# Optimization experiments

Hardware: AMD Instinct MI355X
Metric: run time of the kernel (lower is better)

## Reference

```python
import jax, jax.numpy as jnp
import numpy as np

B, S, H = 1, 2048, 2048
HD, NQ, NKV = 128, 16, 4
FFH = 8192
EPS = 1e-5
ROPE_BASE = 10000.0
SOFTMAX_CAP = 50.0
CLIP_L, CLIP_R = 0.0, 1.0


def setup_inputs() -> dict:
    key = jax.random.key(0)
    ks = jax.random.split(key, 10)
    std = 0.02
    return {
        "x": jax.random.normal(ks[0], (B, S, H), dtype=jnp.float32),
        "attn_norm_w": jax.random.uniform(ks[1], (H,), minval=-1.0, maxval=1.0, dtype=jnp.float32),
        "mlp_norm_w": jax.random.uniform(ks[2], (H,), minval=-1.0, maxval=1.0, dtype=jnp.float32),
        "wq": jax.random.normal(ks[3], (H, NQ * HD), dtype=jnp.float32) * std,
        "wk": jax.random.normal(ks[4], (H, NKV * HD), dtype=jnp.float32) * std,
        "wv": jax.random.normal(ks[5], (H, NKV * HD), dtype=jnp.float32) * std,
        "wo": jax.random.normal(ks[6], (NQ * HD, H), dtype=jnp.float32) * std,
        "w_gate": jax.random.normal(ks[7], (H, FFH), dtype=jnp.float32) * std,
        "w_up": jax.random.normal(ks[8], (H, FFH), dtype=jnp.float32) * std,
        "w_down": jax.random.normal(ks[9], (FFH, H), dtype=jnp.float32) * std,
    }


def _rms_norm(x, w):
    # GroupRMSNorm with group_size=None -> whole hidden dim
    var = jnp.mean(jnp.square(x), axis=-1, keepdims=True)
    return x * jax.lax.rsqrt(var + EPS) * w


def _rope_cos_sin(seq_len, dim):
    inv_freq = 1.0 / (ROPE_BASE ** (jnp.arange(0, dim, 2, dtype=jnp.float32) / dim))
    t = jnp.arange(seq_len, dtype=jnp.float32)
    freqs = jnp.outer(t, inv_freq)                      # [S, dim/2]
    emb = jnp.concatenate([freqs, freqs], axis=-1)      # [S, dim]
    return jnp.cos(emb), jnp.sin(emb)


def _apply_rope(x, cos, sin):
    # x: [B, S, h, d]; rotate-half (LLaMA-style)
    d = x.shape[-1]
    x1, x2 = x[..., : d // 2], x[..., d // 2 :]
    rot = jnp.concatenate([-x2, x1], axis=-1)
    return x * cos[None, :, None, :] + rot * sin[None, :, None, :]


def _qk_norm(x):
    # per-head RMS norm over head_dim (qk_norm_group_size == head_dim), unit weight
    var = jnp.mean(jnp.square(x), axis=-1, keepdims=True)
    return x * jax.lax.rsqrt(var + EPS)


def reference(x, attn_norm_w, mlp_norm_w, wq, wk, wv, wo, w_gate, w_up, w_down):
    # ---- attention sub-layer ----
    h = _rms_norm(x, attn_norm_w)                                     # [B,S,H]
    q = (h @ wq).reshape(B, S, NQ, HD)
    k = (h @ wk).reshape(B, S, NKV, HD)
    v = (h @ wv).reshape(B, S, NKV, HD)

    cos, sin = _rope_cos_sin(S, HD)
    q = _apply_rope(q, cos, sin)
    k = _apply_rope(k, cos, sin)

    q = _qk_norm(q)
    k = _qk_norm(k)

    # GQA: expand kv heads to match q heads
    rep = NQ // NKV
    k = jnp.repeat(k, rep, axis=2)                                    # [B,S,NQ,HD]
    v = jnp.repeat(v, rep, axis=2)

    scale = 1.0 / jnp.sqrt(jnp.float32(HD))
    scores = jnp.einsum("bshd,bthd->bhst", q, k) * scale              # [B,NQ,S,S]
    # softmax cap: cap * tanh(s / cap)
    scores = SOFTMAX_CAP * jnp.tanh(scores / SOFTMAX_CAP)
    causal = jnp.tril(jnp.ones((S, S), dtype=bool))
    scores = jnp.where(causal[None, None], scores, -jnp.inf)
    p = jax.nn.softmax(scores, axis=-1)
    # clip range (l, r): clamp(p * (r - l) + l, 0, 1)
    p = jnp.clip(p * (CLIP_R - CLIP_L) + CLIP_L, 0.0, 1.0)
    o = jnp.einsum("bhst,bthd->bshd", p, v).reshape(B, S, NQ * HD)
    x = x + o @ wo

    # ---- MLP sub-layer (gated SiLU) ----
    h2 = _rms_norm(x, mlp_norm_w)
    mlp_out = (jax.nn.silu(h2 @ w_gate) * (h2 @ w_up)) @ w_down
    return x + mlp_out
```

## Files before the change

kernel.cpp:

```cpp
#include <hip/hip_runtime.h>

typedef __bf16 bf16;
typedef __bf16 bf16x4 __attribute__((ext_vector_type(4)));
typedef __bf16 bf16x8 __attribute__((ext_vector_type(8)));
typedef float f32x4 __attribute__((ext_vector_type(4)));

#define GLP16(gp, lp) __builtin_amdgcn_global_load_lds( \
    (const __attribute__((address_space(1))) void*)(gp), \
    (__attribute__((address_space(3))) void*)(lp), 16, 0, 0)

__device__ __forceinline__ f32x4 mfma16(bf16x8 a, bf16x8 b, f32x4 c) {
    return __builtin_amdgcn_mfma_f32_16x16x32_bf16(a, b, c, 0, 0, 0);
}

__global__ __launch_bounds__(256) void k_rmsnorm(const float* __restrict__ x,
        const float* __restrict__ w, bf16* __restrict__ out) {
    const int H = 2048;
    size_t row = blockIdx.x;
    const float* xr = x + row * H;
    int base = threadIdx.x * 8;
    float4 a = *(const float4*)(xr + base);
    float4 b = *(const float4*)(xr + base + 4);
    float ss = a.x*a.x + a.y*a.y + a.z*a.z + a.w*a.w
             + b.x*b.x + b.y*b.y + b.z*b.z + b.w*b.w;
#pragma unroll
    for (int m = 32; m > 0; m >>= 1) ss += __shfl_xor(ss, m);
    __shared__ float red[4];
    if ((threadIdx.x & 63) == 0) red[threadIdx.x >> 6] = ss;
    __syncthreads();
    float tot = red[0] + red[1] + red[2] + red[3];
    float rs = rsqrtf(tot * (1.0f / H) + 1e-5f);
    float4 wa = *(const float4*)(w + base);
    float4 wb = *(const float4*)(w + base + 4);
    bf16x8 ov;
    ov[0] = (bf16)(a.x * rs * wa.x); ov[1] = (bf16)(a.y * rs * wa.y);
    ov[2] = (bf16)(a.z * rs * wa.z); ov[3] = (bf16)(a.w * rs * wa.w);
    ov[4] = (bf16)(b.x * rs * wb.x); ov[5] = (bf16)(b.y * rs * wb.y);
    ov[6] = (bf16)(b.z * rs * wb.z); ov[7] = (bf16)(b.w * rs * wb.w);
    *(bf16x8*)(out + row * H + base) = ov;
}

__global__ __launch_bounds__(256) void k_convT(const float* __restrict__ W,
        bf16* __restrict__ Wt, int K, int N, int rmul, int roff) {
    __shared__ float t[32][33];
    int k0 = blockIdx.x * 32, n0 = blockIdx.y * 32;
    int tx = threadIdx.x, ty = threadIdx.y;
#pragma unroll
    for (int i = 0; i < 4; i++)
        t[ty + i * 8][tx] = W[(size_t)(k0 + ty + i * 8) * N + n0 + tx];
    __syncthreads();
#pragma unroll
    for (int i = 0; i < 4; i++)
        Wt[((size_t)(n0 + ty + i * 8) * rmul + roff) * K + k0 + tx] =
            (bf16)t[tx][ty + i * 8];
}

__global__ __launch_bounds__(256) void k_transpose(const bf16* __restrict__ in,
        bf16* __restrict__ out, int R, int C) {
    __shared__ bf16 t[32][33];
    int r0 = blockIdx.x * 32, c0 = blockIdx.y * 32;
    int tx = threadIdx.x & 31, ty = threadIdx.x >> 5;
#pragma unroll
    for (int i = 0; i < 4; i++)
        t[ty + i * 8][tx] = in[(size_t)(r0 + ty + i * 8) * C + c0 + tx];
    __syncthreads();
#pragma unroll
    for (int i = 0; i < 4; i++)
        out[(size_t)(c0 + ty + i * 8) * R + r0 + tx] = t[tx][ty + i * 8];
}

template<int EPI>
__global__ __launch_bounds__(512, 2) void k_gemm5(const bf16* __restrict__ A,
        const bf16* __restrict__ Bt, void* __restrict__ outp,
        const void* __restrict__ aux, int M, int N, int K, int ksplit) {
    extern __shared__ char lds[];
    const int tid = threadIdx.x, wave = tid >> 6, lane = tid & 63;
    const int lr = lane & 15, kg = lane >> 4;
    const int wm = wave >> 2, wn = wave & 3;
    const int bn = blockIdx.x, bm = blockIdx.y, split = blockIdx.z;
    const int row0 = bm * 256, col0 = bn * 256;
    const int kbeg = split * ksplit;
    const int NT = ksplit >> 6;
    const size_t K2 = (size_t)K * 2;
    const int xorm = (lr & 7) << 4;

    char* const A0p = lds;
    char* const A1p = lds + 32768;
    char* const B0p = lds + 65536;
    char* const B1p = lds + 98304;

    size_t soff[2];
#pragma unroll
    for (int s = 0; s < 2; s++) {
        int d = s * 8192 + tid * 16;
        int rh = d >> 7, c = d & 127;
        soff[s] = (size_t)rh * K2 + (c ^ ((rh & 7) << 4));
    }
    const char* Ab = (const char*)A + ((size_t)row0 * K + kbeg) * 2;
    const char* Bb = (const char*)Bt + ((size_t)col0 * K + kbeg) * 2;

    auto stA = [&](int t, int mh) {
        const char* src = Ab + (size_t)(mh * 128) * K2 + (size_t)t * 128;
        char* dst = lds + (t & 1) * 32768 + mh * 16384 + wave * 1024;
        GLP16(src + soff[0], dst);
        GLP16(src + soff[1], dst + 8192);
    };
    auto stB = [&](int t, int nh) {
        const char* src = Bb + (size_t)(nh * 128) * K2 + (size_t)t * 128;
        char* dst = lds + 65536 + (t & 1) * 32768 + nh * 16384 + wave * 1024;
        GLP16(src + soff[0], dst);
        GLP16(src + soff[1], dst + 8192);
    };

    f32x4 acc[8][4];
#pragma unroll
    for (int m = 0; m < 8; m++)
#pragma unroll
        for (int n = 0; n < 4; n++) acc[m][n] = (f32x4){0, 0, 0, 0};

    bf16x8 a[8], c0[4], c1[4];
    auto rdA = [&](const char* base, int mh) {
#pragma unroll
        for (int mi = 0; mi < 4; mi++)
#pragma unroll
            for (int kk = 0; kk < 2; kk++) {
                int rh = wm * 64 + mi * 16 + lr;
                int c = (kk * 64 + kg * 16) ^ xorm;
                a[mi * 2 + kk] = *(const bf16x8*)(base + mh * 16384 + rh * 128 + c);
            }
    };
    auto rdB = [&](const char* base, int nh, bf16x8 (&b)[4]) {
#pragma unroll
        for (int nj = 0; nj < 2; nj++)
#pragma unroll
            for (int kk = 0; kk < 2; kk++) {
                int rh = wn * 32 + nj * 16 + lr;
                int c = (kk * 64 + kg * 16) ^ xorm;
                b[nj * 2 + kk] = *(const bf16x8*)(base + nh * 16384 + rh * 128 + c);
            }
    };
    auto mm = [&](int mh, int nh, bf16x8 (&b)[4]) {
#pragma unroll
        for (int mi = 0; mi < 4; mi++)
#pragma unroll
            for (int nj = 0; nj < 2; nj++)
#pragma unroll
                for (int kk = 0; kk < 2; kk++)
                    acc[mh * 4 + mi][nh * 2 + nj] =
                        mfma16(a[mi * 2 + kk], b[nj * 2 + kk],
                               acc[mh * 4 + mi][nh * 2 + nj]);
    };

#define PBAR do { asm volatile("" ::: "memory"); \
                  __builtin_amdgcn_s_barrier(); \
                  asm volatile("" ::: "memory"); } while (0)

    stA(0, 0); stB(0, 0); stB(0, 1); stA(0, 1);
    stA(1, 0); stB(1, 0); stB(1, 1);
    asm volatile("s_waitcnt vmcnt(6)" ::: "memory");
    PBAR;

    const int NIT = NT >> 1;
    for (int it = 0; it < NIT; ++it) {
        const int t = it * 2;
        const bool more = (t + 2 < NT);
        rdA(A0p, 0); rdB(B0p, 0, c0);
        stA(t + 1, 1);
        __builtin_amdgcn_s_setprio(1); mm(0, 0, c0); __builtin_amdgcn_s_setprio(0);
        PBAR;
        rdB(B0p, 1, c1);
        if (more) stA(t + 2, 0);
        __builtin_amdgcn_s_setprio(1); mm(0, 1, c1); __builtin_amdgcn_s_setprio(0);
        PBAR;
        rdA(A0p, 1);
        if (more) stB(t + 2, 0);
        __builtin_amdgcn_s_setprio(1); mm(1, 1, c1); __builtin_amdgcn_s_setprio(0);
        PBAR;
        if (more) stB(t + 2, 1);
        __builtin_amdgcn_s_setprio(1); mm(1, 0, c0); __builtin_amdgcn_s_setprio(0);
        if (more) asm volatile("s_waitcnt vmcnt(6)" ::: "memory");
        else      asm volatile("s_waitcnt vmcnt(0)" ::: "memory");
        PBAR;
        rdA(A1p, 0); rdB(B1p, 0, c0);
        if (more) stA(t + 2, 1);
        __builtin_amdgcn_s_setprio(1); mm(0, 0, c0); __builtin_amdgcn_s_setprio(0);
        PBAR;
        rdB(B1p, 1, c1);
        if (t + 3 < NT) stA(t + 3, 0);
        __builtin_amdgcn_s_setprio(1); mm(0, 1, c1); __builtin_amdgcn_s_setprio(0);
        PBAR;
        rdA(A1p, 1);
        if (t + 3 < NT) stB(t + 3, 0);
        __builtin_amdgcn_s_setprio(1); mm(1, 1, c1); __builtin_amdgcn_s_setprio(0);
        PBAR;
        if (t + 3 < NT) stB(t + 3, 1);
        __builtin_amdgcn_s_setprio(1); mm(1, 0, c0); __builtin_amdgcn_s_setprio(0);
        if (more) asm volatile("s_waitcnt vmcnt(6)" ::: "memory");
        PBAR;
    }
#undef PBAR

#pragma unroll
    for (int mi = 0; mi < 8; mi++)
#pragma unroll
        for (int ni = 0; ni < 4; ni++)
#pragma unroll
            for (int r = 0; r < 4; r++) {
                size_t row = row0 + (mi >> 2) * 128 + wm * 64 + (mi & 3) * 16 + kg * 4 + r;
                size_t col = col0 + (ni >> 1) * 128 + wn * 32 + (ni & 1) * 16 + lr;
                float vv = acc[mi][ni][r];
                if (EPI == 3) {
                    ((float*)outp)[(size_t)split * M * N + row * N + col] = vv;
                } else {
                    float pv = __shfl_xor(vv, 1);
                    float g = (lane & 1) ? pv : vv;
                    float u = (lane & 1) ? vv : pv;
                    float sg = g / (1.0f + __expf(-g));
                    if (!(lane & 1))
                        ((bf16*)outp)[row * (size_t)(N >> 1) + (col >> 1)] =
                            (bf16)(sg * u);
                }
            }
}

__global__ __launch_bounds__(256) void k_reduce(const float* __restrict__ parts,
        const float* __restrict__ resid, float* __restrict__ out,
        int ns, size_t n4) {
    size_t i = (size_t)blockIdx.x * 256 + threadIdx.x;
    if (i >= n4) return;
    float4 acc = ((const float4*)resid)[i];
    for (int s = 0; s < ns; s++) {
        float4 p = ((const float4*)(parts + (size_t)s * n4 * 4))[i];
        acc.x += p.x; acc.y += p.y; acc.z += p.z; acc.w += p.w;
    }
    ((float4*)out)[i] = acc;
}

__global__ __launch_bounds__(256) void k_reduce_rms(const float* __restrict__ parts,
        const float* __restrict__ resid, const float* __restrict__ w,
        float* __restrict__ x2, bf16* __restrict__ hb, int ns) {
    const int H = 2048;
    size_t row = blockIdx.x;
    int base = threadIdx.x * 8;
    const float* rr = resid + row * H + base;
    float4 a = *(const float4*)rr;
    float4 b = *(const float4*)(rr + 4);
    for (int s = 0; s < ns; s++) {
        const float* pp = parts + (size_t)s * H * 2048 + row * H + base;
        float4 pa = *(const float4*)pp;
        float4 pb = *(const float4*)(pp + 4);
        a.x += pa.x; a.y += pa.y; a.z += pa.z; a.w += pa.w;
        b.x += pb.x; b.y += pb.y; b.z += pb.z; b.w += pb.w;
    }
    *(float4*)(x2 + row * H + base) = a;
    *(float4*)(x2 + row * H + base + 4) = b;
    float ss = a.x*a.x + a.y*a.y + a.z*a.z + a.w*a.w
             + b.x*b.x + b.y*b.y + b.z*b.z + b.w*b.w;
#pragma unroll
    for (int m = 32; m > 0; m >>= 1) ss += __shfl_xor(ss, m);
    __shared__ float red[4];
    if ((threadIdx.x & 63) == 0) red[threadIdx.x >> 6] = ss;
    __syncthreads();
    float tot = red[0] + red[1] + red[2] + red[3];
    float rs = rsqrtf(tot * (1.0f / H) + 1e-5f);
    float4 wa = *(const float4*)(w + base);
    float4 wb = *(const float4*)(w + base + 4);
    bf16x8 ov;
    ov[0] = (bf16)(a.x * rs * wa.x); ov[1] = (bf16)(a.y * rs * wa.y);
    ov[2] = (bf16)(a.z * rs * wa.z); ov[3] = (bf16)(a.w * rs * wa.w);
    ov[4] = (bf16)(b.x * rs * wb.x); ov[5] = (bf16)(b.y * rs * wb.y);
    ov[6] = (bf16)(b.z * rs * wb.z); ov[7] = (bf16)(b.w * rs * wb.w);
    *(bf16x8*)(hb + row * H + base) = ov;
}

__global__ __launch_bounds__(256) void k_qkvfin(const float* __restrict__ parts,
        bf16* __restrict__ qb, bf16* __restrict__ kb, bf16* __restrict__ vb) {
    int s = blockIdx.x;
    int col = blockIdx.y * 1024 + threadIdx.x * 4;
    const float* p0 = parts + (size_t)s * 3072 + col;
    const float* p1 = p0 + (size_t)2048 * 3072;
    float4 a = *(const float4*)p0;
    float4 b = *(const float4*)p1;
    a.x += b.x; a.y += b.y; a.z += b.z; a.w += b.w;
    bf16x4 o;
    o[0] = (bf16)a.x; o[1] = (bf16)a.y; o[2] = (bf16)a.z; o[3] = (bf16)a.w;
    if (col < 2048)      *(bf16x4*)(qb + (size_t)s * 2048 + col) = o;
    else if (col < 2560) *(bf16x4*)(kb + (size_t)s * 512 + col - 2048) = o;
    else                 *(bf16x4*)(vb + (size_t)s * 512 + col - 2560) = o;
}

__global__ __launch_bounds__(256) void k_rope(bf16* __restrict__ q,
        bf16* __restrict__ k) {
    int s = blockIdx.x, lane = threadIdx.x & 63;
    int hid = blockIdx.y * 4 + (threadIdx.x >> 6);
    bf16* p;
    if (hid < 16) p = q + (size_t)s * 2048 + hid * 128;
    else          p = k + (size_t)s * 512 + (hid - 16) * 128;
    float x1 = (float)p[lane], x2 = (float)p[lane + 64];
    float f = exp2f((float)lane * -0.2076205059304601f);
    float sn, cs;
    sincosf((float)s * f, &sn, &cs);
    float o1 = x1 * cs - x2 * sn;
    float o2 = x2 * cs + x1 * sn;
    float ss = o1 * o1 + o2 * o2;
#pragma unroll
    for (int m = 32; m > 0; m >>= 1) ss += __shfl_xor(ss, m);
    float rs = rsqrtf(ss * (1.0f / 128.0f) + 1e-5f);
    p[lane] = (bf16)(o1 * rs);
    p[lane + 64] = (bf16)(o2 * rs);
}

__global__ __launch_bounds__(256) void k_attn(const bf16* __restrict__ qg,
        const bf16* __restrict__ kgl, const bf16* __restrict__ vtg,
        bf16* __restrict__ og) {
    extern __shared__ char alds[];
    int pi = blockIdx.x, h = blockIdx.y, kvh = h >> 2;
    int tid = threadIdx.x, wave = tid >> 6, lane = tid & 63;
    int lr = lane & 15, kgrp = lane >> 4;

    int rowQ[4], colQ[4], rowV[4], colV[4];
#pragma unroll
    for (int j = 0; j < 4; j++) {
        int p = j * 4096 + wave * 1024 + lane * 16;
        int ps = p ^ (((p >> 8) & 7) << 4);
        rowQ[j] = ps >> 8; colQ[j] = ps & 255;
        int pv = p ^ (((p >> 7) & 7) << 4);
        rowV[j] = pv >> 7; colV[j] = pv & 127;
    }

    const float C1 = 0.08838834764831845f / 50.0f;
    const float L2E50 = 72.13475204444817f;

#pragma unroll 1
    for (int half = 0; half < 2; ++half) {
        int qt = half ? (31 - pi) : pi;
        int nt = qt + 1;

#pragma unroll
        for (int j = 0; j < 4; j++)
            GLP16((const char*)qg + (size_t)(qt * 64 + rowQ[j]) * 4096 + h * 256 + colQ[j],
                  alds + j * 4096 + wave * 1024);
        for (int t = 0; t < 2 && t < nt; t++) {
#pragma unroll
            for (int j = 0; j < 4; j++)
                GLP16((const char*)kgl + (size_t)(t * 64 + rowQ[j]) * 1024 + kvh * 256 + colQ[j],
                      alds + 16384 + t * 16384 + j * 4096 + wave * 1024);
#pragma unroll
            for (int j = 0; j < 4; j++)
                GLP16((const char*)vtg + (size_t)(kvh * 128 + rowV[j]) * 4096 + t * 128 + colV[j],
                      alds + 49152 + t * 16384 + j * 4096 + wave * 1024);
        }
        if (nt > 1) asm volatile("s_waitcnt vmcnt(8)" ::: "memory");
        else        asm volatile("s_waitcnt vmcnt(0)" ::: "memory");
        __builtin_amdgcn_s_barrier();

        bf16x8 qf[4];
#pragma unroll
        for (int c = 0; c < 4; c++) {
            int b = (wave * 16 + lr) * 256 + c * 64 + kgrp * 16;
            qf[c] = *(const bf16x8*)(alds + (b ^ (((b >> 8) & 7) << 4)));
        }
        f32x4 accO[8];
#pragma unroll
        for (int n = 0; n < 8; n++) accO[n] = (f32x4){0, 0, 0, 0};
        float lsum[4] = {0, 0, 0, 0};
        int qrow = qt * 64 + wave * 16 + kgrp * 4;

        for (int kt = 0; kt < nt; kt++) {
            int buf = kt & 1;
            const char* Kb = alds + 16384 + buf * 16384;
            const char* Vb = alds + 49152 + buf * 16384;
            char* Pb = alds + 81920;
#pragma unroll
            for (int j = 0; j < 4; j++) {
                f32x4 s = {0, 0, 0, 0};
#pragma unroll
                for (int c = 0; c < 4; c++) {
                    int b = (j * 16 + lr) * 256 + c * 64 + kgrp * 16;
                    bf16x8 kf = *(const bf16x8*)(Kb + (b ^ (((b >> 8) & 7) << 4)));
                    s = mfma16(qf[c], kf, s);
                }
                int key = kt * 64 + j * 16 + lr;
#pragma unroll
                for (int r = 0; r < 4; r++) {
                    float y = s[r] * C1;
                    float y2 = y * y;
                    float u = fmaf(y2, 0.13333333f, -0.33333333f);
                    u = fmaf(y2, u, 1.0f);
                    float t5 = y * u;
                    float pe = fmaf(t5, L2E50, -L2E50);
                    float pv = (key <= qrow + r) ? exp2f(pe) : 0.0f;
                    lsum[r] += pv;
                    int wb = (wave * 16 + kgrp * 4 + r) * 128 + (j * 16 + lr) * 2;
                    *(bf16*)(Pb + (wb ^ (((wb >> 7) & 7) << 4))) = (bf16)pv;
                }
            }
            bf16x8 pf[2];
#pragma unroll
            for (int ks2 = 0; ks2 < 2; ks2++) {
                int b = (wave * 16 + lr) * 128 + ks2 * 64 + kgrp * 16;
                pf[ks2] = *(const bf16x8*)(Pb + (b ^ (((b >> 7) & 7) << 4)));
            }
#pragma unroll
            for (int n = 0; n < 8; n++)
#pragma unroll
                for (int ks2 = 0; ks2 < 2; ks2++) {
                    int b = (n * 16 + lr) * 128 + ks2 * 64 + kgrp * 16;
                    bf16x8 vf = *(const bf16x8*)(Vb + (b ^ (((b >> 7) & 7) << 4)));
                    accO[n] = mfma16(pf[ks2], vf, accO[n]);
                }
            __builtin_amdgcn_s_barrier();
            bool more = (kt + 2 < nt);
            if (more) {
                int t = kt + 2;
#pragma unroll
                for (int j = 0; j < 4; j++)
                    GLP16((const char*)kgl + (size_t)(t * 64 + rowQ[j]) * 1024 + kvh * 256 + colQ[j],
                          alds + 16384 + buf * 16384 + j * 4096 + wave * 1024);
#pragma unroll
                for (int j = 0; j < 4; j++)
                    GLP16((const char*)vtg + (size_t)(kvh * 128 + rowV[j]) * 4096 + t * 128 + colV[j],
                          alds + 49152 + buf * 16384 + j * 4096 + wave * 1024);
            }
            if (kt + 1 < nt) {
                if (more) asm volatile("s_waitcnt vmcnt(8)" ::: "memory");
                else      asm volatile("s_waitcnt vmcnt(0)" ::: "memory");
                __builtin_amdgcn_s_barrier();
            }
        }
#pragma unroll
        for (int r = 0; r < 4; r++) {
            float t = lsum[r];
            t += __shfl_xor(t, 1); t += __shfl_xor(t, 2);
            t += __shfl_xor(t, 4); t += __shfl_xor(t, 8);
            lsum[r] = t;
        }
#pragma unroll
        for (int n = 0; n < 8; n++)
#pragma unroll
            for (int r = 0; r < 4; r++) {
                size_t row = qt * 64 + wave * 16 + kgrp * 4 + r;
                og[row * 2048 + h * 128 + n * 16 + lr] = (bf16)(accO[n][r] / lsum[r]);
            }
    }
}

extern "C" void kernel_launch(void* const* d_in, const int* in_sizes, int n_in,
                              void* d_out, int out_size, void* d_ws, size_t ws_size,
                              hipStream_t stream) {
    const float* x      = (const float*)d_in[0];
    const float* attn_w = (const float*)d_in[1];
    const float* mlp_w  = (const float*)d_in[2];
    const float* wq     = (const float*)d_in[3];
    const float* wk     = (const float*)d_in[4];
    const float* wv     = (const float*)d_in[5];
    const float* wo     = (const float*)d_in[6];
    const float* wgate  = (const float*)d_in[7];
    const float* wup    = (const float*)d_in[8];
    const float* wdown  = (const float*)d_in[9];
    float* out = (float*)d_out;
    char* ws = (char*)d_ws;

    const size_t MB = 1024 * 1024;
    bf16* Wqkv = (bf16*)(ws + 0);
    bf16* vt   = (bf16*)(ws + 0);
    float* pO  = (float*)(ws + 0);
    bf16* Wgu  = (bf16*)(ws + 0);
    float* pD  = (float*)(ws + 0);
    bf16* WoT  = (bf16*)(ws + 64 * MB);
    bf16* WdT  = (bf16*)(ws + 64 * MB);
    bf16* hb   = (bf16*)(ws + 96 * MB);
    bf16* qb   = (bf16*)(ws + 104 * MB);
    bf16* kb   = (bf16*)(ws + 112 * MB);
    bf16* vb   = (bf16*)(ws + 114 * MB);
    bf16* ob   = (bf16*)(ws + 116 * MB);
    float* x2  = (float*)(ws + 124 * MB);
    bf16* gb   = (bf16*)(ws + 140 * MB);
    float* pQ  = (float*)(ws + 116 * MB);

    const int LDS5 = 131072;
    hipFuncSetAttribute((const void*)&k_gemm5<3>,
        hipFuncAttributeMaxDynamicSharedMemorySize, LDS5);
    hipFuncSetAttribute((const void*)&k_gemm5<4>,
        hipFuncAttributeMaxDynamicSharedMemorySize, LDS5);
    const int LDSA = 90112;
    hipFuncSetAttribute((const void*)&k_attn,
        hipFuncAttributeMaxDynamicSharedMemorySize, LDSA);

    dim3 cb(32, 8);
    const size_t n4 = (size_t)2048 * 2048 / 4;

    k_rmsnorm<<<2048, 256, 0, stream>>>(x, attn_w, hb);
    k_convT<<<dim3(64, 64), cb, 0, stream>>>(wq, Wqkv, 2048, 2048, 1, 0);
    k_convT<<<dim3(64, 16), cb, 0, stream>>>(wk, Wqkv + 4194304, 2048, 512, 1, 0);
    k_convT<<<dim3(64, 16), cb, 0, stream>>>(wv, Wqkv + 5242880, 2048, 512, 1, 0);
    k_gemm5<3><<<dim3(12, 8, 2), 512, LDS5, stream>>>(hb, Wqkv, pQ, nullptr,
                                                      2048, 3072, 2048, 1024);
    k_qkvfin<<<dim3(2048, 3), 256, 0, stream>>>(pQ, qb, kb, vb);
    k_transpose<<<dim3(64, 16), 256, 0, stream>>>(vb, vt, 2048, 512);
    k_rope<<<dim3(2048, 5), 256, 0, stream>>>(qb, kb);
    k_attn<<<dim3(16, 16), 256, LDSA, stream>>>(qb, kb, vt, ob);
    k_convT<<<dim3(64, 64), cb, 0, stream>>>(wo, WoT, 2048, 2048, 1, 0);
    k_gemm5<3><<<dim3(8, 8, 4), 512, LDS5, stream>>>(ob, WoT, pO, nullptr,
                                                     2048, 2048, 2048, 512);
    k_reduce_rms<<<2048, 256, 0, stream>>>(pO, x, mlp_w, x2, hb, 4);
    k_convT<<<dim3(64, 256), cb, 0, stream>>>(wgate, Wgu, 2048, 8192, 2, 0);
    k_convT<<<dim3(64, 256), cb, 0, stream>>>(wup, Wgu, 2048, 8192, 2, 1);
    k_gemm5<4><<<dim3(64, 8, 1), 512, LDS5, stream>>>(hb, Wgu, gb, nullptr,
                                                      2048, 16384, 2048, 2048);
    k_convT<<<dim3(256, 64), cb, 0, stream>>>(wdown, WdT, 8192, 2048, 1, 0);
    k_gemm5<3><<<dim3(8, 8, 4), 512, LDS5, stream>>>(gb, WdT, pD, nullptr,
                                                     2048, 2048, 8192, 2048);
    k_reduce<<<4096, 256, 0, stream>>>(pD, x2, out, 4, n4);
}
```

Measured before the change: 467.0 us.

## Store split-K partials in bf16 and split attention into one q-tile per block

Split-K GEMM partial sums for QKV, Wo and down projections are now written as bf16 instead of fp32, and the reduce kernels read bf16x8. This halves the partial-sum write and read traffic, at some cost in precision. Separately, the attention kernel no longer loops over two paired q-tiles per block. It launches twice as many blocks, each handling one tile, with launch_bounds(256,2). The P buffer now reuses the Q region of LDS, which cuts dynamic LDS from 90 KB to 80 KB to allow two blocks per CU.

Result: no change. 463.4 us (-0.8%).

```diff
diff --git a/kernel.cpp b/kernel.cpp
--- a/kernel.cpp
+++ b/kernel.cpp
@@ -209,8 +209,8 @@
                 size_t row = row0 + (mi >> 2) * 128 + wm * 64 + (mi & 3) * 16 + kg * 4 + r;
                 size_t col = col0 + (ni >> 1) * 128 + wn * 32 + (ni & 1) * 16 + lr;
                 float vv = acc[mi][ni][r];
-                if (EPI == 3) {
-                    ((float*)outp)[(size_t)split * M * N + row * N + col] = vv;
+                if (EPI == 5) {
+                    ((bf16*)outp)[(size_t)split * M * N + row * N + col] = (bf16)vv;
                 } else {
                     float pv = __shfl_xor(vv, 1);
                     float g = (lane & 1) ? pv : vv;
@@ -223,20 +223,24 @@
             }
 }
 
-__global__ __launch_bounds__(256) void k_reduce(const float* __restrict__ parts,
+__global__ __launch_bounds__(256) void k_reduce(const bf16* __restrict__ parts,
         const float* __restrict__ resid, float* __restrict__ out,
-        int ns, size_t n4) {
+        int ns, size_t n8) {
     size_t i = (size_t)blockIdx.x * 256 + threadIdx.x;
-    if (i >= n4) return;
-    float4 acc = ((const float4*)resid)[i];
+    if (i >= n8) return;
+    size_t base = i * 8;
+    float4 a = *(const float4*)(resid + base);
+    float4 b = *(const float4*)(resid + base + 4);
     for (int s = 0; s < ns; s++) {
-        float4 p = ((const float4*)(parts + (size_t)s * n4 * 4))[i];
-        acc.x += p.x; acc.y += p.y; acc.z += p.z; acc.w += p.w;
-    }
-    ((float4*)out)[i] = acc;
-}
-
-__global__ __launch_bounds__(256) void k_reduce_rms(const float* __restrict__ parts,
+        bf16x8 p = *(const bf16x8*)(parts + (size_t)s * n8 * 8 + base);
+        a.x += (float)p[0]; a.y += (float)p[1]; a.z += (float)p[2]; a.w += (float)p[3];
+        b.x += (float)p[4]; b.y += (float)p[5]; b.z += (float)p[6]; b.w += (float)p[7];
+    }
+    *(float4*)(out + base) = a;
+    *(float4*)(out + base + 4) = b;
+}
+
+__global__ __launch_bounds__(256) void k_reduce_rms(const bf16* __restrict__ parts,
         const float* __restrict__ resid, const float* __restrict__ w,
         float* __restrict__ x2, bf16* __restrict__ hb, int ns) {
     const int H = 2048;
@@ -246,11 +250,9 @@
     float4 a = *(const float4*)rr;
     float4 b = *(const float4*)(rr + 4);
     for (int s = 0; s < ns; s++) {
-        const float* pp = parts + (size_t)s * H * 2048 + row * H + base;
-        float4 pa = *(const float4*)pp;
-        float4 pb = *(const float4*)(pp + 4);
-        a.x += pa.x; a.y += pa.y; a.z += pa.z; a.w += pa.w;
-        b.x += pb.x; b.y += pb.y; b.z += pb.z; b.w += pb.w;
+        bf16x8 p = *(const bf16x8*)(parts + (size_t)s * H * 2048 + row * H + base);
+        a.x += (float)p[0]; a.y += (float)p[1]; a.z += (float)p[2]; a.w += (float)p[3];
+        b.x += (float)p[4]; b.y += (float)p[5]; b.z += (float)p[6]; b.w += (float)p[7];
     }
     *(float4*)(x2 + row * H + base) = a;
     *(float4*)(x2 + row * H + base + 4) = b;
@@ -273,17 +275,17 @@
     *(bf16x8*)(hb + row * H + base) = ov;
 }
 
-__global__ __launch_bounds__(256) void k_qkvfin(const float* __restrict__ parts,
+__global__ __launch_bounds__(256) void k_qkvfin(const bf16* __restrict__ parts,
         bf16* __restrict__ qb, bf16* __restrict__ kb, bf16* __restrict__ vb) {
     int s = blockIdx.x;
     int col = blockIdx.y * 1024 + threadIdx.x * 4;
-    const float* p0 = parts + (size_t)s * 3072 + col;
-    const float* p1 = p0 + (size_t)2048 * 3072;
-    float4 a = *(const float4*)p0;
-    float4 b = *(const float4*)p1;
-    a.x += b.x; a.y += b.y; a.z += b.z; a.w += b.w;
+    const bf16* p0 = parts + (size_t)s * 3072 + col;
+    const bf16* p1 = p0 + (size_t)2048 * 3072;
+    bf16x4 a = *(const bf16x4*)p0;
+    bf16x4 b = *(const bf16x4*)p1;
     bf16x4 o;
-    o[0] = (bf16)a.x; o[1] = (bf16)a.y; o[2] = (bf16)a.z; o[3] = (bf16)a.w;
+#pragma unroll
+    for (int j = 0; j < 4; j++) o[j] = (bf16)((float)a[j] + (float)b[j]);
     if (col < 2048)      *(bf16x4*)(qb + (size_t)s * 2048 + col) = o;
     else if (col < 2560) *(bf16x4*)(kb + (size_t)s * 512 + col - 2048) = o;
     else                 *(bf16x4*)(vb + (size_t)s * 512 + col - 2560) = o;
@@ -310,11 +312,13 @@
     p[lane + 64] = (bf16)(o2 * rs);
 }
 
-__global__ __launch_bounds__(256) void k_attn(const bf16* __restrict__ qg,
+__global__ __launch_bounds__(256, 2) void k_attn(const bf16* __restrict__ qg,
         const bf16* __restrict__ kgl, const bf16* __restrict__ vtg,
         bf16* __restrict__ og) {
     extern __shared__ char alds[];
     int pi = blockIdx.x, h = blockIdx.y, kvh = h >> 2;
+    int qt = (pi & 1) ? (31 - (pi >> 1)) : (pi >> 1);
+    int nt = qt + 1;
     int tid = threadIdx.x, wave = tid >> 6, lane = tid & 63;
     int lr = lane & 15, kgrp = lane >> 4;
 
@@ -331,118 +335,114 @@
     const float C1 = 0.08838834764831845f / 50.0f;
     const float L2E50 = 72.13475204444817f;
 
-#pragma unroll 1
-    for (int half = 0; half < 2; ++half) {
-        int qt = half ? (31 - pi) : pi;
-        int nt = qt + 1;
-
+#pragma unroll
+    for (int j = 0; j < 4; j++)
+        GLP16((const char*)qg + (size_t)(qt * 64 + rowQ[j]) * 4096 + h * 256 + colQ[j],
+              alds + j * 4096 + wave * 1024);
+    for (int t = 0; t < 2 && t < nt; t++) {
 #pragma unroll
         for (int j = 0; j < 4; j++)
-            GLP16((const char*)qg + (size_t)(qt * 64 + rowQ[j]) * 4096 + h * 256 + colQ[j],
-                  alds + j * 4096 + wave * 1024);
-        for (int t = 0; t < 2 && t < nt; t++) {
+            GLP16((const char*)kgl + (size_t)(t * 64 + rowQ[j]) * 1024 + kvh * 256 + colQ[j],
+                  alds + 16384 + t * 16384 + j * 4096 + wave * 1024);
+#pragma unroll
+        for (int j = 0; j < 4; j++)
+            GLP16((const char*)vtg + (size_t)(kvh * 128 + rowV[j]) * 4096 + t * 128 + colV[j],
+                  alds + 49152 + t * 16384 + j * 4096 + wave * 1024);
+    }
+    if (nt > 1) asm volatile("s_waitcnt vmcnt(8)" ::: "memory");
+    else        asm volatile("s_waitcnt vmcnt(0)" ::: "memory");
+    __builtin_amdgcn_s_barrier();
+
+    bf16x8 qf[4];
+#pragma unroll
+    for (int c = 0; c < 4; c++) {
+        int b = (wave * 16 + lr) * 256 + c * 64 + kgrp * 16;
+        qf[c] = *(const bf16x8*)(alds + (b ^ (((b >> 8) & 7) << 4)));
+    }
+    __builtin_amdgcn_s_barrier();
+
+    f32x4 accO[8];
+#pragma unroll
+    for (int n = 0; n < 8; n++) accO[n] = (f32x4){0, 0, 0, 0};
+    float lsum[4] = {0, 0, 0, 0};
+    int qrow = qt * 64 + wave * 16 + kgrp * 4;
+
+    for (int kt = 0; kt < nt; kt++) {
+        int buf = kt & 1;
+        const char* Kb = alds + 16384 + buf * 16384;
+        const char* Vb = alds + 49152 + buf * 16384;
+        char* Pb = alds;
+#pragma unroll
+        for (int j = 0; j < 4; j++) {
+            f32x4 s = {0, 0, 0, 0};
+#pragma unroll
+            for (int c = 0; c < 4; c++) {
+                int b = (j * 16 + lr) * 256 + c * 64 + kgrp * 16;
+                bf16x8 kf = *(const bf16x8*)(Kb + (b ^ (((b >> 8) & 7) << 4)));
+                s = mfma16(qf[c], kf, s);
+            }
+            int key = kt * 64 + j * 16 + lr;
+#pragma unroll
+            for (int r = 0; r < 4; r++) {
+                float y = s[r] * C1;
+                float y2 = y * y;
+                float u = fmaf(y2, 0.13333333f, -0.33333333f);
+                u = fmaf(y2, u, 1.0f);
+                float t5 = y * u;
+                float pe = fmaf(t5, L2E50, -L2E50);
+                float pv = (key <= qrow + r) ? exp2f(pe) : 0.0f;
+                lsum[r] += pv;
+                int wb = (wave * 16 + kgrp * 4 + r) * 128 + (j * 16 + lr) * 2;
+                *(bf16*)(Pb + (wb ^ (((wb >> 7) & 7) << 4))) = (bf16)pv;
+            }
+        }
+        bf16x8 pf[2];
+#pragma unroll
+        for (int ks2 = 0; ks2 < 2; ks2++) {
+            int b = (wave * 16 + lr) * 128 + ks2 * 64 + kgrp * 16;
+            pf[ks2] = *(const bf16x8*)(Pb + (b ^ (((b >> 7) & 7) << 4)));
+        }
+#pragma unroll
+        for (int n = 0; n < 8; n++)
+#pragma unroll
+            for (int ks2 = 0; ks2 < 2; ks2++) {
+                int b = (n * 16 + lr) * 128 + ks2 * 64 + kgrp * 16;
+                bf16x8 vf = *(const bf16x8*)(Vb + (b ^ (((b >> 7) & 7) << 4)));
+                accO[n] = mfma16(pf[ks2], vf, accO[n]);
+            }
+        __builtin_amdgcn_s_barrier();
+        bool more = (kt + 2 < nt);
+        if (more) {
+            int t = kt + 2;
 #pragma unroll
             for (int j = 0; j < 4; j++)
                 GLP16((const char*)kgl + (size_t)(t * 64 + rowQ[j]) * 1024 + kvh * 256 + colQ[j],
-                      alds + 16384 + t * 16384 + j * 4096 + wave * 1024);
+                      alds + 16384 + buf * 16384 + j * 4096 + wave * 1024);
 #pragma unroll
             for (int j = 0; j < 4; j++)
                 GLP16((const char*)vtg + (size_t)(kvh * 128 + rowV[j]) * 4096 + t * 128 + colV[j],
-                      alds + 49152 + t * 16384 + j * 4096 + wave * 1024);
+                      alds + 49152 + buf * 16384 + j * 4096 + wave * 1024);
         }
-        if (nt > 1) asm volatile("s_waitcnt vmcnt(8)" ::: "memory");
-        else        asm volatile("s_waitcnt vmcnt(0)" ::: "memory");
-        __builtin_amdgcn_s_barrier();
-
-        bf16x8 qf[4];
-#pragma unroll
-        for (int c = 0; c < 4; c++) {
-            int b = (wave * 16 + lr) * 256 + c * 64 + kgrp * 16;
-            qf[c] = *(const bf16x8*)(alds + (b ^ (((b >> 8) & 7) << 4)));
+        if (kt + 1 < nt) {
+            if (more) asm volatile("s_waitcnt vmcnt(8)" ::: "memory");
+            else      asm volatile("s_waitcnt vmcnt(0)" ::: "memory");
+            __builtin_amdgcn_s_barrier();
         }
-        f32x4 accO[8];
-#pragma unroll
-        for (int n = 0; n < 8; n++) accO[n] = (f32x4){0, 0, 0, 0};
-        float lsum[4] = {0, 0, 0, 0};
-        int qrow = qt * 64 + wave * 16 + kgrp * 4;
-
-        for (int kt = 0; kt < nt; kt++) {
-            int buf = kt & 1;
-            const char* Kb = alds + 16384 + buf * 16384;
-            const char* Vb = alds + 49152 + buf * 16384;
-            char* Pb = alds + 81920;
-#pragma unroll
-            for (int j = 0; j < 4; j++) {
-                f32x4 s = {0, 0, 0, 0};
-#pragma unroll
-                for (int c = 0; c < 4; c++) {
-                    int b = (j * 16 + lr) * 256 + c * 64 + kgrp * 16;
-                    bf16x8 kf = *(const bf16x8*)(Kb + (b ^ (((b >> 8) & 7) << 4)));
-                    s = mfma16(qf[c], kf, s);
-                }
-                int key = kt * 64 + j * 16 + lr;
-#pragma unroll
-                for (int r = 0; r < 4; r++) {
-                    float y = s[r] * C1;
-                    float y2 = y * y;
-                    float u = fmaf(y2, 0.13333333f, -0.33333333f);
-                    u = fmaf(y2, u, 1.0f);
-                    float t5 = y * u;
-                    float pe = fmaf(t5, L2E50, -L2E50);
-                    float pv = (key <= qrow + r) ? exp2f(pe) : 0.0f;
-                    lsum[r] += pv;
-                    int wb = (wave * 16 + kgrp * 4 + r) * 128 + (j * 16 + lr) * 2;
-                    *(bf16*)(Pb + (wb ^ (((wb >> 7) & 7) << 4))) = (bf16)pv;
-                }
-            }
-            bf16x8 pf[2];
-#pragma unroll
-            for (int ks2 = 0; ks2 < 2; ks2++) {
-                int b = (wave * 16 + lr) * 128 + ks2 * 64 + kgrp * 16;
-                pf[ks2] = *(const bf16x8*)(Pb + (b ^ (((b >> 7) & 7) << 4)));
-            }
-#pragma unroll
-            for (int n = 0; n < 8; n++)
-#pragma unroll
-                for (int ks2 = 0; ks2 < 2; ks2++) {
-                    int b = (n * 16 + lr) * 128 + ks2 * 64 + kgrp * 16;
-                    bf16x8 vf = *(const bf16x8*)(Vb + (b ^ (((b >> 7) & 7) << 4)));
-                    accO[n] = mfma16(pf[ks2], vf, accO[n]);
-                }
-            __builtin_amdgcn_s_barrier();
-            bool more = (kt + 2 < nt);
-            if (more) {
-                int t = kt + 2;
-#pragma unroll
-                for (int j = 0; j < 4; j++)
-                    GLP16((const char*)kgl + (size_t)(t * 64 + rowQ[j]) * 1024 + kvh * 256 + colQ[j],
-                          alds + 16384 + buf * 16384 + j * 4096 + wave * 1024);
-#pragma unroll
-                for (int j = 0; j < 4; j++)
-                    GLP16((const char*)vtg + (size_t)(kvh * 128 + rowV[j]) * 4096 + t * 128 + colV[j],
-                          alds + 49152 + buf * 16384 + j * 4096 + wave * 1024);
-            }
-            if (kt + 1 < nt) {
-                if (more) asm volatile("s_waitcnt vmcnt(8)" ::: "memory");
-                else      asm volatile("s_waitcnt vmcnt(0)" ::: "memory");
-                __builtin_amdgcn_s_barrier();
-            }
+    }
+#pragma unroll
+    for (int r = 0; r < 4; r++) {
+        float t = lsum[r];
+        t += __shfl_xor(t, 1); t += __shfl_xor(t, 2);
+        t += __shfl_xor(t, 4); t += __shfl_xor(t, 8);
+        lsum[r] = t;
+    }
+#pragma unroll
+    for (int n = 0; n < 8; n++)
+#pragma unroll
+        for (int r = 0; r < 4; r++) {
+            size_t row = qt * 64 + wave * 16 + kgrp * 4 + r;
+            og[row * 2048 + h * 128 + n * 16 + lr] = (bf16)(accO[n][r] / lsum[r]);
         }
-#pragma unroll
-        for (int r = 0; r < 4; r++) {
-            float t = lsum[r];
-            t += __shfl_xor(t, 1); t += __shfl_xor(t, 2);
-            t += __shfl_xor(t, 4); t += __shfl_xor(t, 8);
-            lsum[r] = t;
-        }
-#pragma unroll
-        for (int n = 0; n < 8; n++)
-#pragma unroll
-            for (int r = 0; r < 4; r++) {
-                size_t row = qt * 64 + wave * 16 + kgrp * 4 + r;
-                og[row * 2048 + h * 128 + n * 16 + lr] = (bf16)(accO[n][r] / lsum[r]);
-            }
-    }
 }
 
 extern "C" void kernel_launch(void* const* d_in, const int* in_sizes, int n_in,
@@ -464,9 +464,9 @@
     const size_t MB = 1024 * 1024;
     bf16* Wqkv = (bf16*)(ws + 0);
     bf16* vt   = (bf16*)(ws + 0);
-    float* pO  = (float*)(ws + 0);
+    bf16* pO   = (bf16*)(ws + 0);
     bf16* Wgu  = (bf16*)(ws + 0);
-    float* pD  = (float*)(ws + 0);
+    bf16* pD   = (bf16*)(ws + 0);
     bf16* WoT  = (bf16*)(ws + 64 * MB);
     bf16* WdT  = (bf16*)(ws + 64 * MB);
     bf16* hb   = (bf16*)(ws + 96 * MB);
@@ -476,32 +476,33 @@
     bf16* ob   = (bf16*)(ws + 116 * MB);
     float* x2  = (float*)(ws + 124 * MB);
     bf16* gb   = (bf16*)(ws + 140 * MB);
-    float* pQ  = (float*)(ws + 116 * MB);
+    bf16* pQ   = (bf16*)(ws + 116 * MB);
+    pQ = (bf16*)(ws + 172 * MB);
 
     const int LDS5 = 131072;
-    hipFuncSetAttribute((const void*)&k_gemm5<3>,
-        hipFuncAttributeMaxDynamicSharedMemorySize, LDS5);
     hipFuncSetAttribute((const void*)&k_gemm5<4>,
         hipFuncAttributeMaxDynamicSharedMemorySize, LDS5);
-    const int LDSA = 90112;
+    hipFuncSetAttribute((const void*)&k_gemm5<5>,
+        hipFuncAttributeMaxDynamicSharedMemorySize, LDS5);
+    const int LDSA = 81920;
     hipFuncSetAttribute((const void*)&k_attn,
         hipFuncAttributeMaxDynamicSharedMemorySize, LDSA);
 
     dim3 cb(32, 8);
-    const size_t n4 = (size_t)2048 * 2048 / 4;
+    const size_t n8 = (size_t)2048 * 2048 / 8;
 
     k_rmsnorm<<<2048, 256, 0, stream>>>(x, attn_w, hb);
     k_convT<<<dim3(64, 64), cb, 0, stream>>>(wq, Wqkv, 2048, 2048, 1, 0);
     k_convT<<<dim3(64, 16), cb, 0, stream>>>(wk, Wqkv + 4194304, 2048, 512, 1, 0);
     k_convT<<<dim3(64, 16), cb, 0, stream>>>(wv, Wqkv + 5242880, 2048, 512, 1, 0);
-    k_gemm5<3><<<dim3(12, 8, 2), 512, LDS5, stream>>>(hb, Wqkv, pQ, nullptr,
+    k_gemm5<5><<<dim3(12, 8, 2), 512, LDS5, stream>>>(hb, Wqkv, pQ, nullptr,
                                                       2048, 3072, 2048, 1024);
     k_qkvfin<<<dim3(2048, 3), 256, 0, stream>>>(pQ, qb, kb, vb);
     k_transpose<<<dim3(64, 16), 256, 0, stream>>>(vb, vt, 2048, 512);
     k_rope<<<dim3(2048, 5), 256, 0, stream>>>(qb, kb);
-    k_attn<<<dim3(16, 16), 256, LDSA, stream>>>(qb, kb, vt, ob);
+    k_attn<<<dim3(32, 16), 256, LDSA, stream>>>(qb, kb, vt, ob);
     k_convT<<<dim3(64, 64), cb, 0, stream>>>(wo, WoT, 2048, 2048, 1, 0);
-    k_gemm5<3><<<dim3(8, 8, 4), 512, LDS5, stream>>>(ob, WoT, pO, nullptr,
+    k_gemm5<5><<<dim3(8, 8, 4), 512, LDS5, stream>>>(ob, WoT, pO, nullptr,
                                                      2048, 2048, 2048, 512);
     k_reduce_rms<<<2048, 256, 0, stream>>>(pO, x, mlp_w, x2, hb, 4);
     k_convT<<<dim3(64, 256), cb, 0, stream>>>(wgate, Wgu, 2048, 8192, 2, 0);
@@ -509,7 +510,7 @@
     k_gemm5<4><<<dim3(64, 8, 1), 512, LDS5, stream>>>(hb, Wgu, gb, nullptr,
                                                       2048, 16384, 2048, 2048);
     k_convT<<<dim3(256, 64), cb, 0, stream>>>(wdown, WdT, 8192, 2048, 1, 0);
-    k_gemm5<3><<<dim3(8, 8, 4), 512, LDS5, stream>>>(gb, WdT, pD, nullptr,
+    k_gemm5<5><<<dim3(8, 8, 4), 512, LDS5, stream>>>(gb, WdT, pD, nullptr,
                                                      2048, 2048, 8192, 2048);
-    k_reduce<<<4096, 256, 0, stream>>>(pD, x2, out, 4, n4);
-}
+    k_reduce<<<2048, 256, 0, stream>>>(pD, x2, out, 4, n8);
+}
```
